# Kernel tuning notes

Hardware: AMD Instinct MI355X
Metric: run time of the kernel (lower is better)

## Reference

```python
import jax, jax.numpy as jnp
import numpy as np

D_IN = 64   # T (condition_length)
D = 128     # latent_dim
H = 8       # num_head
N = 2       # batch of graphs
M = 512     # num_nodes
T_OBS = 5.0


def leaky(v):
    return jnp.where(v >= 0, v, 0.2 * v)


def setup_inputs() -> dict:
    key = jax.random.key(0)
    ks = jax.random.split(key, 24)
    g = lambda k, s: jax.random.normal(k, s, dtype=jnp.float32) * 0.05
    return {
        "x": jax.random.normal(ks[0], (N, M, D_IN), dtype=jnp.float32),
        # f_node: T -> 2D -> D
        "fn_w1": g(ks[1], (D_IN, 2 * D)), "fn_b1": g(ks[2], (2 * D,)),
        "fn_w2": g(ks[3], (2 * D, D)),   "fn_b2": g(ks[4], (D,)),
        # per-head K/Q/V projections, stacked over heads
        "wk": g(ks[5], (H, D, D)), "bk": g(ks[6], (H, D)),
        "wq": g(ks[7], (H, D, D)), "bq": g(ks[8], (H, D)),
        "wv": g(ks[9], (H, D, D)), "bv": g(ks[10], (H, D)),
        # f_v: H*D -> D -> D
        "fv_w1": g(ks[11], (H * D, D)), "fv_b1": g(ks[12], (D,)),
        "fv_w2": g(ks[13], (D, D)),     "fv_b2": g(ks[14], (D,)),
        # f_node2edge: 2D -> D -> 1
        "fe_w1": g(ks[15], (2 * D, D)), "fe_b1": g(ks[16], (D,)),
        "fe_w2": g(ks[17], (D, 1)),     "fe_b2": g(ks[18], (1,)),
    }


def reference(x, fn_w1, fn_b1, fn_w2, fn_b2, wk, bk, wq, bq, wv, bv,
              fv_w1, fv_b1, fv_w2, fv_b2, fe_w1, fe_b1, fe_w2, fe_b2):
    n, m, T = x.shape
    # TemporalEncoding with d_hid=1: div_term = [1.0], even col -> sin(t)
    t = jnp.linspace(0.0, T_OBS, T)
    te = jnp.sin(t)  # [T]
    # f_node
    h = jax.nn.relu((x + te) @ fn_w1 + fn_b1) @ fn_w2 + fn_b2  # [N,M,D]
    # per-head attention (sender=K_i, receiver=Q_j -> scores = K Q^T)
    K = jnp.einsum('nmd,hde->hnme', h, wk) + bk[:, None, None, :]
    Q = jnp.einsum('nmd,hde->hnme', h, wq) + bq[:, None, None, :]
    V = jnp.einsum('nmd,hde->hnme', h, wv) + bv[:, None, None, :]
    scores = jnp.einsum('hnid,hnjd->hnij', K, Q)           # [H,N,M,M]
    alpha = jax.nn.softmax(leaky(scores), axis=-1)
    att = leaky(jnp.einsum('hnij,hnjd->hnid', alpha, V))   # [H,N,M,D]
    # concat heads along feature dim (head 0 first)
    att = jnp.transpose(att, (1, 2, 0, 3)).reshape(n, m, -1)  # [N,M,H*D]
    x2 = jax.nn.relu(att @ fv_w1 + fv_b1) @ fv_w2 + fv_b2 + h  # [N,M,D]
    # pairwise node2edge FFN: pair(i,j) = concat(x2_i, x2_j)
    half = fe_w1.shape[0] // 2
    A = x2 @ fe_w1[:half]   # contribution of node i
    B = x2 @ fe_w1[half:]   # contribution of node j
    hid = jax.nn.relu(A[:, :, None, :] + B[:, None, :, :] + fe_b1)  # [N,M,M,D]
    edge = (hid @ fe_w2 + fe_b2)[..., 0] / float(m)  # [N,M,M]
    return (x2, edge)
```

## Files before the change

kernel.cpp:

```cpp
#include <hip/hip_runtime.h>

typedef unsigned short u16;
typedef unsigned int u32;
typedef __attribute__((ext_vector_type(8))) short short8;
typedef __attribute__((ext_vector_type(4))) float f32x4;

__device__ __forceinline__ u16 f2b(float f) {
  union { float f; u32 i; } v; v.f = f;
  u32 i = v.i;
  return (u16)((i + 0x7FFFu + ((i >> 16) & 1u)) >> 16);
}
__device__ __forceinline__ float lo16(u32 x) { union { u32 i; float f; } v; v.i = x << 16; return v.f; }
__device__ __forceinline__ float hi16(u32 x) { union { u32 i; float f; } v; v.i = x & 0xffff0000u; return v.f; }
__device__ __forceinline__ u32 pack2(float a, float b) { return (u32)f2b(a) | ((u32)f2b(b) << 16); }

__device__ __align__(16) float g_h[1024 * 128];
__device__ __align__(16) u16   g_hb[1024 * 128];
__device__ __align__(16) u16   g_Wt[24 * 128 * 128];
__device__ __align__(16) u16   g_w1t[128 * 1024];
__device__ __align__(16) u16   g_w2t[128 * 128];
__device__ __align__(16) u16   g_fat[2 * 128 * 128];
__device__ __align__(16) u16   g_K[16 * 512 * 128];
__device__ __align__(16) u16   g_Q[16 * 512 * 128];
__device__ __align__(16) u16   g_V[16 * 512 * 128];
__device__ __align__(16) u16   g_Opb[512 * 64 * 128];
__device__ __align__(16) float g_ml[512 * 64 * 2];
__device__ __align__(16) float g_A[1024 * 128];
__device__ __align__(16) float g_Bm[1024 * 128];

__global__ void k_fnode(const float* __restrict__ x, const float* __restrict__ w1,
                        const float* __restrict__ b1, const float* __restrict__ w2,
                        const float* __restrict__ b2, const float* __restrict__ wk,
                        const float* __restrict__ wq, const float* __restrict__ wv,
                        const float* __restrict__ fvw1, const float* __restrict__ fvw2,
                        const float* __restrict__ few1) {
  __shared__ float xr[2 * 64];
  __shared__ float hids[2 * 256];
  __shared__ float red[2048];
  int tx = threadIdx.x;
  int row0 = blockIdx.x * 2;
  if (tx < 128) {
    int r = tx >> 6, k = tx & 63;
    xr[tx] = x[(row0 + r) * 64 + k] + sinf((float)k * (5.0f / 63.0f));
  }
  {
    int base = blockIdx.x * 1280 + tx;
#pragma unroll
    for (int t = 0; t < 5; t++) {
      int idx = base + t * 256;
      if (idx < 393216) {
        int ph = idx >> 14, rem = idx & 16383, e = rem >> 7, d = rem & 127;
        int proj = ph >> 3, head = ph & 7;
        const float* W = (proj == 0) ? wk : (proj == 1) ? wq : wv;
        g_Wt[idx] = f2b(W[head * 16384 + d * 128 + e]);
      } else if (idx < 524288) {
        int idx2 = idx - 393216;
        int e = idx2 >> 10, k = idx2 & 1023;
        g_w1t[idx2] = f2b(fvw1[k * 128 + e]);
      } else if (idx < 540672) {
        int idx3 = idx - 524288;
        int e = idx3 >> 7, k = idx3 & 127;
        g_w2t[idx3] = f2b(fvw2[k * 128 + e]);
      } else if (idx < 573440) {
        int idx4 = idx - 540672;
        int half = idx4 >> 14, rem = idx4 & 16383;
        int e = rem >> 7, k = rem & 127;
        g_fat[idx4] = f2b(few1[(half * 128 + k) * 128 + e]);
      }
    }
  }
  __syncthreads();
  {
    int ks = tx >> 6, cg = tx & 63;
    float acc[2][4] = {};
#pragma unroll 4
    for (int i = 0; i < 16; i++) {
      int k = ks * 16 + i;
      float4 w4 = *(const float4*)&w1[k * 256 + cg * 4];
      float a0 = xr[k], a1 = xr[64 + k];
      acc[0][0] = fmaf(a0, w4.x, acc[0][0]); acc[0][1] = fmaf(a0, w4.y, acc[0][1]);
      acc[0][2] = fmaf(a0, w4.z, acc[0][2]); acc[0][3] = fmaf(a0, w4.w, acc[0][3]);
      acc[1][0] = fmaf(a1, w4.x, acc[1][0]); acc[1][1] = fmaf(a1, w4.y, acc[1][1]);
      acc[1][2] = fmaf(a1, w4.z, acc[1][2]); acc[1][3] = fmaf(a1, w4.w, acc[1][3]);
    }
#pragma unroll
    for (int r = 0; r < 2; r++)
      *(float4*)&red[ks * 512 + r * 256 + cg * 4] = *(float4*)acc[r];
  }
  __syncthreads();
#pragma unroll
  for (int jo = 0; jo < 2; jo++) {
    int o = jo * 256 + tx;
    float s = red[o] + red[512 + o] + red[1024 + o] + red[1536 + o];
    hids[o] = fmaxf(s + b1[o & 255], 0.0f);
  }
  __syncthreads();
  {
    int ks = tx >> 5, eg = tx & 31;
    float acc[2][4] = {};
#pragma unroll 4
    for (int i = 0; i < 32; i++) {
      int k = ks * 32 + i;
      float4 w4 = *(const float4*)&w2[k * 128 + eg * 4];
      float a0 = hids[k], a1 = hids[256 + k];
      acc[0][0] = fmaf(a0, w4.x, acc[0][0]); acc[0][1] = fmaf(a0, w4.y, acc[0][1]);
      acc[0][2] = fmaf(a0, w4.z, acc[0][2]); acc[0][3] = fmaf(a0, w4.w, acc[0][3]);
      acc[1][0] = fmaf(a1, w4.x, acc[1][0]); acc[1][1] = fmaf(a1, w4.y, acc[1][1]);
      acc[1][2] = fmaf(a1, w4.z, acc[1][2]); acc[1][3] = fmaf(a1, w4.w, acc[1][3]);
    }
    __syncthreads();
#pragma unroll
    for (int r = 0; r < 2; r++)
      *(float4*)&red[ks * 256 + r * 128 + eg * 4] = *(float4*)acc[r];
  }
  __syncthreads();
  {
    float s = 0.0f;
#pragma unroll
    for (int ks = 0; ks < 8; ks++) s += red[ks * 256 + tx];
    int r = tx >> 7, e = tx & 127;
    float v = s + b2[e];
    g_h[(row0 + r) * 128 + e] = v;
    g_hb[(row0 + r) * 128 + e] = f2b(v);
  }
}

__global__ __launch_bounds__(256) void k_kqv(
    const float* __restrict__ bk, const float* __restrict__ bq,
    const float* __restrict__ bv) {
  __shared__ u16 hs[64 * 136];
  __shared__ u16 Wt[128 * 136];
  int b = blockIdx.x, tx = threadIdx.x;
  int rt = b & 15, ph = b >> 4;
  int proj = ph >> 3, head = ph & 7;
  const float* Bb = (proj == 0) ? bk : (proj == 1) ? bq : bv;
  u16* O = (proj == 0) ? g_K : (proj == 1) ? g_Q : g_V;
  int r0 = rt * 64;
#pragma unroll
  for (int t = 0; t < 4; t++) {
    int idx = t * 256 + tx, row = idx >> 4, oct = idx & 15;
    *(uint4*)&hs[row * 136 + oct * 8] = *(const uint4*)&g_hb[(r0 + row) * 128 + oct * 8];
  }
  const u16* Wtg = g_Wt + ph * 16384;
#pragma unroll
  for (int t = 0; t < 8; t++) {
    int idx = t * 256 + tx, row = idx >> 4, oct = idx & 15;
    *(uint4*)&Wt[row * 136 + oct * 8] = *(const uint4*)&Wtg[row * 128 + oct * 8];
  }
  __syncthreads();
  int lane = tx & 63, wv_ = tx >> 6, cl = lane & 15, quad = lane >> 4;
  short8 bH[4];
#pragma unroll
  for (int kk = 0; kk < 4; kk++)
    bH[kk] = *(const short8*)&hs[(wv_ * 16 + cl) * 136 + kk * 32 + quad * 8];
  f32x4 zero = {0.0f, 0.0f, 0.0f, 0.0f};
  f32x4 acc[8];
#pragma unroll
  for (int em = 0; em < 8; em++) acc[em] = zero;
#pragma unroll
  for (int em = 0; em < 8; em++)
#pragma unroll
    for (int kk = 0; kk < 4; kk++) {
      short8 aW = *(const short8*)&Wt[(em * 16 + cl) * 136 + kk * 32 + quad * 8];
      acc[em] = __builtin_amdgcn_mfma_f32_16x16x32_bf16(aW, bH[kk], acc[em], 0, 0, 0);
    }
#pragma unroll
  for (int em = 0; em < 8; em++) {
    float4 b4 = *(const float4*)&Bb[head * 128 + em * 16 + quad * 4];
    uint2 st = make_uint2(pack2(acc[em][0] + b4.x, acc[em][1] + b4.y),
                          pack2(acc[em][2] + b4.z, acc[em][3] + b4.w));
    *(uint2*)&O[(head * 1024 + r0 + wv_ * 16 + cl) * 128 + em * 16 + quad * 4] = st;
  }
}

__global__ __launch_bounds__(256) void k_attn() {
  __shared__ u16 Ks[64 * 136];
  __shared__ u16 Qs[64 * 136];
  __shared__ u16 Vt[128 * 72];
  __shared__ u16 Pw[4 * 16 * 72];
  __shared__ float alphas[4 * 16];
  int b = blockIdx.x, tx = threadIdx.x;
  int jc = b & 3, it = (b >> 2) & 7, hn = b >> 5;
  int i0 = it * 64;
  const u16* Kp = g_K + hn * 65536;
  const u16* Qp = g_Q + hn * 65536;
  const u16* Vp = g_V + hn * 65536;
#pragma unroll
  for (int t = 0; t < 4; t++) {
    int idx = t * 256 + tx, row = idx >> 4, oct = idx & 15;
    *(uint4*)&Ks[row * 136 + oct * 8] = *(const uint4*)&Kp[(i0 + row) * 128 + oct * 8];
  }
  int lane = tx & 63, wv = tx >> 6;
  int cl = lane & 15, quad = lane >> 4;
  f32x4 zero = {0.0f, 0.0f, 0.0f, 0.0f};
  f32x4 o[8];
#pragma unroll
  for (int es = 0; es < 8; es++) o[es] = zero;
  float m_ = -1e30f, l_ = 0.0f;

  for (int jt = 0; jt < 2; jt++) {
    int j0 = jc * 128 + jt * 64;
    __syncthreads();
#pragma unroll
    for (int t = 0; t < 4; t++) {
      int idx = t * 256 + tx, row = idx >> 4, oct = idx & 15;
      *(uint4*)&Qs[row * 136 + oct * 8] = *(const uint4*)&Qp[(j0 + row) * 128 + oct * 8];
    }
    {
      int jg = (tx & 15) * 4, e8 = (tx >> 4) * 8;
      uint4 r0 = *(const uint4*)&Vp[(j0 + jg + 0) * 128 + e8];
      uint4 r1 = *(const uint4*)&Vp[(j0 + jg + 1) * 128 + e8];
      uint4 r2 = *(const uint4*)&Vp[(j0 + jg + 2) * 128 + e8];
      uint4 r3 = *(const uint4*)&Vp[(j0 + jg + 3) * 128 + e8];
      const u32* p0 = (const u32*)&r0; const u32* p1 = (const u32*)&r1;
      const u32* p2 = (const u32*)&r2; const u32* p3 = (const u32*)&r3;
#pragma unroll
      for (int c = 0; c < 8; c++) {
        int w = c >> 1, sh = (c & 1) * 16;
        u32 lo = ((p0[w] >> sh) & 0xffffu) | (((p1[w] >> sh) & 0xffffu) << 16);
        u32 hi = ((p2[w] >> sh) & 0xffffu) | (((p3[w] >> sh) & 0xffffu) << 16);
        *(uint2*)&Vt[(e8 + c) * 72 + jg] = make_uint2(lo, hi);
      }
    }
    __syncthreads();
    short8 bK[4];
#pragma unroll
    for (int kk = 0; kk < 4; kk++)
      bK[kk] = *(const short8*)&Ks[(wv * 16 + cl) * 136 + kk * 32 + quad * 8];
    f32x4 st[4];
#pragma unroll
    for (int s = 0; s < 4; s++) {
      f32x4 acc = zero;
#pragma unroll
      for (int kk = 0; kk < 4; kk++) {
        short8 aQ = *(const short8*)&Qs[(s * 16 + cl) * 136 + kk * 32 + quad * 8];
        acc = __builtin_amdgcn_mfma_f32_16x16x32_bf16(aQ, bK[kk], acc, 0, 0, 0);
      }
      st[s] = acc;
    }
    float p[4][4];
    float tm = -1e30f;
#pragma unroll
    for (int s = 0; s < 4; s++)
#pragma unroll
      for (int r = 0; r < 4; r++) {
        float v = st[s][r];
        v = fmaxf(v, 0.2f * v);
        p[s][r] = v;
        tm = fmaxf(tm, v);
      }
    tm = fmaxf(tm, __shfl_xor(tm, 16));
    tm = fmaxf(tm, __shfl_xor(tm, 32));
    float mn = fmaxf(m_, tm);
    float alpha = __expf(m_ - mn);
    m_ = mn;
    float ps = 0.0f;
#pragma unroll
    for (int s = 0; s < 4; s++)
#pragma unroll
      for (int r = 0; r < 4; r++) {
        float e = __expf(p[s][r] - mn);
        p[s][r] = e;
        ps += e;
      }
    ps += __shfl_xor(ps, 16);
    ps += __shfl_xor(ps, 32);
    l_ = l_ * alpha + ps;
#pragma unroll
    for (int s = 0; s < 4; s++) {
      uint2 w2v = make_uint2(pack2(p[s][0], p[s][1]), pack2(p[s][2], p[s][3]));
      *(uint2*)&Pw[(wv * 16 + cl) * 72 + s * 16 + quad * 4] = w2v;
    }
    if (quad == 0) alphas[wv * 16 + cl] = alpha;
    __syncthreads();
    f32x4 av = *(const f32x4*)&alphas[wv * 16 + quad * 4];
#pragma unroll
    for (int es = 0; es < 8; es++) o[es] *= av;
    short8 aP[2];
#pragma unroll
    for (int k2 = 0; k2 < 2; k2++)
      aP[k2] = *(const short8*)&Pw[(wv * 16 + cl) * 72 + k2 * 32 + quad * 8];
#pragma unroll
    for (int es = 0; es < 8; es++) {
#pragma unroll
      for (int k2 = 0; k2 < 2; k2++) {
        short8 bV = *(const short8*)&Vt[(es * 16 + cl) * 72 + k2 * 32 + quad * 8];
        o[es] = __builtin_amdgcn_mfma_f32_16x16x32_bf16(aP[k2], bV, o[es], 0, 0, 0);
      }
    }
  }
#pragma unroll
  for (int es = 0; es < 8; es++)
#pragma unroll
    for (int r = 0; r < 4; r++)
      g_Opb[(b * 64 + wv * 16 + quad * 4 + r) * 128 + es * 16 + cl] = f2b(o[es][r]);
  if (quad == 0) {
    g_ml[(b * 64 + wv * 16 + cl) * 2 + 0] = m_;
    g_ml[(b * 64 + wv * 16 + cl) * 2 + 1] = l_;
  }
}

__global__ __launch_bounds__(256) void k_fv(
    const float* __restrict__ fv_b1, const float* __restrict__ fv_b2,
    const float* __restrict__ fe_b1, float* __restrict__ x2out) {
  __shared__ u16 atts[16 * 1032];
  __shared__ u16 wst[128 * 136];
  __shared__ u16 hidb[16 * 136];
  __shared__ u16 x2b[16 * 136];
  int b = blockIdx.x, tx = threadIdx.x;
  int r0 = b * 16;

  {
    int task = tx >> 1, half = tx & 1;
    int lr = task >> 3, head = task & 7;
    int gr = r0 + lr;
    int n = gr >> 9, i = gr & 511;
    int it = i >> 6, lr64 = i & 63;
    int hn = head * 2 + n;
    int mlbase = (hn * 32 + it * 4) * 64 + lr64;
    float mc[4], lc[4];
#pragma unroll
    for (int c = 0; c < 4; c++) {
      float2 ml = *(const float2*)&g_ml[(mlbase + c * 64) * 2];
      mc[c] = ml.x; lc[c] = ml.y;
    }
    float ms = fmaxf(fmaxf(mc[0], mc[1]), fmaxf(mc[2], mc[3]));
    float lsum = 0.0f;
    float ra[64];
#pragma unroll
    for (int i2 = 0; i2 < 64; i2++) ra[i2] = 0.0f;
#pragma unroll
    for (int c = 0; c < 4; c++) {
      float w = __expf(mc[c] - ms);
      lsum += w * lc[c];
      const u16* src = &g_Opb[(mlbase + c * 64) * 128 + half * 64];
#pragma unroll
      for (int ov = 0; ov < 8; ov++) {
        uint4 v = *(const uint4*)&src[ov * 8];
        ra[ov * 8 + 0] = fmaf(w, lo16(v.x), ra[ov * 8 + 0]);
        ra[ov * 8 + 1] = fmaf(w, hi16(v.x), ra[ov * 8 + 1]);
        ra[ov * 8 + 2] = fmaf(w, lo16(v.y), ra[ov * 8 + 2]);
        ra[ov * 8 + 3] = fmaf(w, hi16(v.y), ra[ov * 8 + 3]);
        ra[ov * 8 + 4] = fmaf(w, lo16(v.z), ra[ov * 8 + 4]);
        ra[ov * 8 + 5] = fmaf(w, hi16(v.z), ra[ov * 8 + 5]);
        ra[ov * 8 + 6] = fmaf(w, lo16(v.w), ra[ov * 8 + 6]);
        ra[ov * 8 + 7] = fmaf(w, hi16(v.w), ra[ov * 8 + 7]);
      }
    }
    float inv = 1.0f / lsum;
    u32 pk[32];
#pragma unroll
    for (int i2 = 0; i2 < 32; i2++) {
      float v0 = ra[i2 * 2] * inv;     v0 = fmaxf(v0, 0.2f * v0);
      float v1 = ra[i2 * 2 + 1] * inv; v1 = fmaxf(v1, 0.2f * v1);
      pk[i2] = pack2(v0, v1);
    }
    int dst = lr * 1032 + head * 128 + half * 64;
#pragma unroll
    for (int ov = 0; ov < 8; ov++)
      *(uint4*)&atts[dst + ov * 8] =
          make_uint4(pk[ov * 4], pk[ov * 4 + 1], pk[ov * 4 + 2], pk[ov * 4 + 3]);
  }
  __syncthreads();

  int lane = tx & 63, w = tx >> 6, cl = lane & 15, quad = lane >> 4;
  f32x4 zero = {0.0f, 0.0f, 0.0f, 0.0f};

  f32x4 accH[2] = {zero, zero};
  for (int kc = 0; kc < 8; kc++) {
#pragma unroll
    for (int q = 0; q < 8; q++) {
      int idx = q * 256 + tx, row = idx >> 4, oct = idx & 15;
      *(uint4*)&wst[row * 136 + oct * 8] =
          *(const uint4*)&g_w1t[row * 1024 + kc * 128 + oct * 8];
    }
    __syncthreads();
    short8 bA[4];
#pragma unroll
    for (int kk = 0; kk < 4; kk++)
      bA[kk] = *(const short8*)&atts[cl * 1032 + kc * 128 + kk * 32 + quad * 8];
#pragma unroll
    for (int t2 = 0; t2 < 2; t2++) {
      int em = 2 * w + t2;
#pragma unroll
      for (int kk = 0; kk < 4; kk++) {
        short8 aW = *(const short8*)&wst[(em * 16 + cl) * 136 + kk * 32 + quad * 8];
        accH[t2] = __builtin_amdgcn_mfma_f32_16x16x32_bf16(aW, bA[kk], accH[t2], 0, 0, 0);
      }
    }
    __syncthreads();
  }

#pragma unroll
  for (int t2 = 0; t2 < 2; t2++) {
    int eb = (2 * w + t2) * 16 + quad * 4;
    float4 b4 = *(const float4*)&fv_b1[eb];
    float v0 = fmaxf(accH[t2][0] + b4.x, 0.0f);
    float v1 = fmaxf(accH[t2][1] + b4.y, 0.0f);
    float v2 = fmaxf(accH[t2][2] + b4.z, 0.0f);
    float v3 = fmaxf(accH[t2][3] + b4.w, 0.0f);
    *(u32*)&hidb[cl * 136 + eb] = pack2(v0, v1);
    *(u32*)&hidb[cl * 136 + eb + 2] = pack2(v2, v3);
  }
#pragma unroll
  for (int q = 0; q < 8; q++) {
    int idx = q * 256 + tx, row = idx >> 4, oct = idx & 15;
    *(uint4*)&wst[row * 136 + oct * 8] = *(const uint4*)&g_w2t[row * 128 + oct * 8];
  }
  __syncthreads();

  {
    short8 bH2[4];
#pragma unroll
    for (int kk = 0; kk < 4; kk++)
      bH2[kk] = *(const short8*)&hidb[cl * 136 + kk * 32 + quad * 8];
    int gr = r0 + cl;
#pragma unroll
    for (int t2 = 0; t2 < 2; t2++) {
      int em = 2 * w + t2;
      f32x4 acc2 = zero;
#pragma unroll
      for (int kk = 0; kk < 4; kk++) {
        short8 aW = *(const short8*)&wst[(em * 16 + cl) * 136 + kk * 32 + quad * 8];
        acc2 = __builtin_amdgcn_mfma_f32_16x16x32_bf16(aW, bH2[kk], acc2, 0, 0, 0);
      }
      int eb = em * 16 + quad * 4;
      float4 b4 = *(const float4*)&fv_b2[eb];
      float4 h4 = *(const float4*)&g_h[gr * 128 + eb];
      float4 xv;
      xv.x = acc2[0] + b4.x + h4.x;
      xv.y = acc2[1] + b4.y + h4.y;
      xv.z = acc2[2] + b4.z + h4.z;
      xv.w = acc2[3] + b4.w + h4.w;
      *(float4*)&x2out[gr * 128 + eb] = xv;
      *(u32*)&x2b[cl * 136 + eb] = pack2(xv.x, xv.y);
      *(u32*)&x2b[cl * 136 + eb + 2] = pack2(xv.z, xv.w);
    }
  }
  __syncthreads();

#pragma unroll
  for (int q = 0; q < 8; q++) {
    int idx = q * 256 + tx, row = idx >> 4, oct = idx & 15;
    *(uint4*)&wst[row * 136 + oct * 8] = *(const uint4*)&g_fat[row * 128 + oct * 8];
  }
  __syncthreads();
  short8 bX[4];
#pragma unroll
  for (int kk = 0; kk < 4; kk++)
    bX[kk] = *(const short8*)&x2b[cl * 136 + kk * 32 + quad * 8];
  {
    int gr = r0 + cl;
#pragma unroll
    for (int t2 = 0; t2 < 2; t2++) {
      int em = 2 * w + t2;
      f32x4 accA = zero;
#pragma unroll
      for (int kk = 0; kk < 4; kk++) {
        short8 aW = *(const short8*)&wst[(em * 16 + cl) * 136 + kk * 32 + quad * 8];
        accA = __builtin_amdgcn_mfma_f32_16x16x32_bf16(aW, bX[kk], accA, 0, 0, 0);
      }
      int eb = em * 16 + quad * 4;
      float4 b4 = *(const float4*)&fe_b1[eb];
      float4 av;
      av.x = accA[0] + b4.x; av.y = accA[1] + b4.y;
      av.z = accA[2] + b4.z; av.w = accA[3] + b4.w;
      *(float4*)&g_A[gr * 128 + eb] = av;
    }
  }
  __syncthreads();

#pragma unroll
  for (int q = 0; q < 8; q++) {
    int idx = q * 256 + tx, row = idx >> 4, oct = idx & 15;
    *(uint4*)&wst[row * 136 + oct * 8] =
        *(const uint4*)&g_fat[16384 + row * 128 + oct * 8];
  }
  __syncthreads();
  {
    int gr = r0 + cl;
#pragma unroll
    for (int t2 = 0; t2 < 2; t2++) {
      int em = 2 * w + t2;
      f32x4 accB = zero;
#pragma unroll
      for (int kk = 0; kk < 4; kk++) {
        short8 aW = *(const short8*)&wst[(em * 16 + cl) * 136 + kk * 32 + quad * 8];
        accB = __builtin_amdgcn_mfma_f32_16x16x32_bf16(aW, bX[kk], accB, 0, 0, 0);
      }
      int eb = em * 16 + quad * 4;
      *(f32x4*)&g_Bm[gr * 128 + eb] = accB;
    }
  }
}

__global__ void k_edge(const float* __restrict__ few2, const float* __restrict__ feb2,
                       float* __restrict__ edge) {
  __shared__ float As[4 * 128];
  __shared__ float w2s[128];
  int b = blockIdx.x, tx = threadIdx.x;
  int n = b >> 8, rest = b & 255, ig = rest >> 1, jh = rest & 1;
  int i0 = ig * 4;
  if (tx < 128) w2s[tx] = few2[tx];
  As[tx] = g_A[(n * 512 + i0) * 128 + tx];
  As[tx + 256] = g_A[(n * 512 + i0) * 128 + tx + 256];
  float eb2 = feb2[0];
  __syncthreads();
  int j = jh * 256 + tx;
  const float* B0 = &g_Bm[(n * 512 + j) * 128];
  float acc[4] = {};
#pragma unroll 4
  for (int dc = 0; dc < 32; dc++) {
    float4 bv = *(const float4*)&B0[dc * 4];
    float4 w4 = *(const float4*)&w2s[dc * 4];
#pragma unroll
    for (int i = 0; i < 4; i++) {
      float4 a4 = *(const float4*)&As[i * 128 + dc * 4];
      acc[i] = fmaf(fmaxf(a4.x + bv.x, 0.0f), w4.x, acc[i]);
      acc[i] = fmaf(fmaxf(a4.y + bv.y, 0.0f), w4.y, acc[i]);
      acc[i] = fmaf(fmaxf(a4.z + bv.z, 0.0f), w4.z, acc[i]);
      acc[i] = fmaf(fmaxf(a4.w + bv.w, 0.0f), w4.w, acc[i]);
    }
  }
  const float scale = 1.0f / 512.0f;
#pragma unroll
  for (int i = 0; i < 4; i++)
    edge[(n * 512 + i0 + i) * 512 + j] = (acc[i] + eb2) * scale;
}

extern "C" void kernel_launch(void* const* d_in, const int* in_sizes, int n_in,
                              void* d_out, int out_size, void* d_ws, size_t ws_size,
                              hipStream_t stream) {
  (void)in_sizes; (void)n_in; (void)out_size; (void)d_ws; (void)ws_size;
  const float* x     = (const float*)d_in[0];
  const float* fn_w1 = (const float*)d_in[1];
  const float* fn_b1 = (const float*)d_in[2];
  const float* fn_w2 = (const float*)d_in[3];
  const float* fn_b2 = (const float*)d_in[4];
  const float* wk    = (const float*)d_in[5];
  const float* bk    = (const float*)d_in[6];
  const float* wq    = (const float*)d_in[7];
  const float* bq    = (const float*)d_in[8];
  const float* wv    = (const float*)d_in[9];
  const float* bv    = (const float*)d_in[10];
  const float* fv_w1 = (const float*)d_in[11];
  const float* fv_b1 = (const float*)d_in[12];
  const float* fv_w2 = (const float*)d_in[13];
  const float* fv_b2 = (const float*)d_in[14];
  const float* fe_w1 = (const float*)d_in[15];
  const float* fe_b1 = (const float*)d_in[16];
  const float* fe_w2 = (const float*)d_in[17];
  const float* fe_b2 = (const float*)d_in[18];

  float* x2out = (float*)d_out;
  float* edge  = x2out + 131072;

  k_fnode<<<512, 256, 0, stream>>>(x, fn_w1, fn_b1, fn_w2, fn_b2, wk, wq, wv,
                                   fv_w1, fv_w2, fe_w1);
  k_kqv<<<384, 256, 0, stream>>>(bk, bq, bv);
  k_attn<<<512, 256, 0, stream>>>();
  k_fv<<<64, 256, 0, stream>>>(fv_b1, fv_b2, fe_b1, x2out);
  k_edge<<<512, 256, 0, stream>>>(fe_w2, fe_b2, edge);
}
```

Measured before the change: 144.1 us.

## Fuse K/Q/V projection into attention kernel and widen fv kernel to 512 threads

Removes the separate K/Q/V projection kernel. The attention kernel now computes its K tile, and the Q and V tiles for each j-chunk, directly from bf16 h and the weights into shared memory, which drops the K/Q/V global round trip and one launch. The price is recomputation: Q and V are projected once per i-tile (8x redundant) and K once per j-chunk (4x). The fv kernel moves to 512 threads with one 16-column tile per wave and reads weights straight from global memory instead of staging them through shared memory, cutting syncs.

```diff
diff --git a/kernel.cpp b/kernel.cpp
--- a/kernel.cpp
+++ b/kernel.cpp
@@ -20,9 +20,6 @@
 __device__ __align__(16) u16   g_w1t[128 * 1024];
 __device__ __align__(16) u16   g_w2t[128 * 128];
 __device__ __align__(16) u16   g_fat[2 * 128 * 128];
-__device__ __align__(16) u16   g_K[16 * 512 * 128];
-__device__ __align__(16) u16   g_Q[16 * 512 * 128];
-__device__ __align__(16) u16   g_V[16 * 512 * 128];
 __device__ __align__(16) u16   g_Opb[512 * 64 * 128];
 __device__ __align__(16) float g_ml[512 * 64 * 2];
 __device__ __align__(16) float g_A[1024 * 128];
@@ -125,74 +122,53 @@
   }
 }
 
-__global__ __launch_bounds__(256) void k_kqv(
+__global__ __launch_bounds__(256) void k_qattn(
     const float* __restrict__ bk, const float* __restrict__ bq,
     const float* __restrict__ bv) {
-  __shared__ u16 hs[64 * 136];
-  __shared__ u16 Wt[128 * 136];
-  int b = blockIdx.x, tx = threadIdx.x;
-  int rt = b & 15, ph = b >> 4;
-  int proj = ph >> 3, head = ph & 7;
-  const float* Bb = (proj == 0) ? bk : (proj == 1) ? bq : bv;
-  u16* O = (proj == 0) ? g_K : (proj == 1) ? g_Q : g_V;
-  int r0 = rt * 64;
-#pragma unroll
-  for (int t = 0; t < 4; t++) {
-    int idx = t * 256 + tx, row = idx >> 4, oct = idx & 15;
-    *(uint4*)&hs[row * 136 + oct * 8] = *(const uint4*)&g_hb[(r0 + row) * 128 + oct * 8];
-  }
-  const u16* Wtg = g_Wt + ph * 16384;
-#pragma unroll
-  for (int t = 0; t < 8; t++) {
-    int idx = t * 256 + tx, row = idx >> 4, oct = idx & 15;
-    *(uint4*)&Wt[row * 136 + oct * 8] = *(const uint4*)&Wtg[row * 128 + oct * 8];
-  }
-  __syncthreads();
-  int lane = tx & 63, wv_ = tx >> 6, cl = lane & 15, quad = lane >> 4;
-  short8 bH[4];
-#pragma unroll
-  for (int kk = 0; kk < 4; kk++)
-    bH[kk] = *(const short8*)&hs[(wv_ * 16 + cl) * 136 + kk * 32 + quad * 8];
-  f32x4 zero = {0.0f, 0.0f, 0.0f, 0.0f};
-  f32x4 acc[8];
-#pragma unroll
-  for (int em = 0; em < 8; em++) acc[em] = zero;
-#pragma unroll
-  for (int em = 0; em < 8; em++)
-#pragma unroll
-    for (int kk = 0; kk < 4; kk++) {
-      short8 aW = *(const short8*)&Wt[(em * 16 + cl) * 136 + kk * 32 + quad * 8];
-      acc[em] = __builtin_amdgcn_mfma_f32_16x16x32_bf16(aW, bH[kk], acc[em], 0, 0, 0);
-    }
-#pragma unroll
-  for (int em = 0; em < 8; em++) {
-    float4 b4 = *(const float4*)&Bb[head * 128 + em * 16 + quad * 4];
-    uint2 st = make_uint2(pack2(acc[em][0] + b4.x, acc[em][1] + b4.y),
-                          pack2(acc[em][2] + b4.z, acc[em][3] + b4.w));
-    *(uint2*)&O[(head * 1024 + r0 + wv_ * 16 + cl) * 128 + em * 16 + quad * 4] = st;
-  }
-}
-
-__global__ __launch_bounds__(256) void k_attn() {
-  __shared__ u16 Ks[64 * 136];
+  __shared__ union { u16 Ks[64 * 136]; u16 Pw[64 * 72]; } kp;
   __shared__ u16 Qs[64 * 136];
   __shared__ u16 Vt[128 * 72];
-  __shared__ u16 Pw[4 * 16 * 72];
-  __shared__ float alphas[4 * 16];
+  __shared__ float alphas[64];
   int b = blockIdx.x, tx = threadIdx.x;
   int jc = b & 3, it = (b >> 2) & 7, hn = b >> 5;
+  int head = hn >> 1, n = hn & 1;
   int i0 = it * 64;
-  const u16* Kp = g_K + hn * 65536;
-  const u16* Qp = g_Q + hn * 65536;
-  const u16* Vp = g_V + hn * 65536;
-#pragma unroll
-  for (int t = 0; t < 4; t++) {
-    int idx = t * 256 + tx, row = idx >> 4, oct = idx & 15;
-    *(uint4*)&Ks[row * 136 + oct * 8] = *(const uint4*)&Kp[(i0 + row) * 128 + oct * 8];
-  }
-  int lane = tx & 63, wv = tx >> 6;
-  int cl = lane & 15, quad = lane >> 4;
+  int lane = tx & 63, wv = tx >> 6, cl = lane & 15, quad = lane >> 4;
+  const u16* WtK = g_Wt + (head) * 16384;
+  const u16* WtQ = g_Wt + (8 + head) * 16384;
+  const u16* WtV = g_Wt + (16 + head) * 16384;
   f32x4 zero = {0.0f, 0.0f, 0.0f, 0.0f};
+
+  {
+    const u16* hbK = &g_hb[(n * 512 + i0 + wv * 16 + cl) * 128];
+    short8 bH[4];
+#pragma unroll
+    for (int kk = 0; kk < 4; kk++)
+      bH[kk] = *(const short8*)&hbK[kk * 32 + quad * 8];
+    f32x4 acc[8];
+#pragma unroll
+    for (int em = 0; em < 8; em++) acc[em] = zero;
+#pragma unroll
+    for (int em = 0; em < 8; em++)
+#pragma unroll
+      for (int kk = 0; kk < 4; kk++) {
+        short8 aW = *(const short8*)&WtK[(em * 16 + cl) * 128 + kk * 32 + quad * 8];
+        acc[em] = __builtin_amdgcn_mfma_f32_16x16x32_bf16(aW, bH[kk], acc[em], 0, 0, 0);
+      }
+#pragma unroll
+    for (int em = 0; em < 8; em++) {
+      float4 b4 = *(const float4*)&bk[head * 128 + em * 16 + quad * 4];
+      int addr = (wv * 16 + cl) * 136 + em * 16 + quad * 4;
+      *(u32*)&kp.Ks[addr] = pack2(acc[em][0] + b4.x, acc[em][1] + b4.y);
+      *(u32*)&kp.Ks[addr + 2] = pack2(acc[em][2] + b4.z, acc[em][3] + b4.w);
+    }
+  }
+  __syncthreads();
+  short8 bK[4];
+#pragma unroll
+  for (int kk = 0; kk < 4; kk++)
+    bK[kk] = *(const short8*)&kp.Ks[(wv * 16 + cl) * 136 + kk * 32 + quad * 8];
+
   f32x4 o[8];
 #pragma unroll
   for (int es = 0; es < 8; es++) o[es] = zero;
@@ -201,32 +177,57 @@
   for (int jt = 0; jt < 2; jt++) {
     int j0 = jc * 128 + jt * 64;
     __syncthreads();
-#pragma unroll
-    for (int t = 0; t < 4; t++) {
-      int idx = t * 256 + tx, row = idx >> 4, oct = idx & 15;
-      *(uint4*)&Qs[row * 136 + oct * 8] = *(const uint4*)&Qp[(j0 + row) * 128 + oct * 8];
-    }
     {
-      int jg = (tx & 15) * 4, e8 = (tx >> 4) * 8;
-      uint4 r0 = *(const uint4*)&Vp[(j0 + jg + 0) * 128 + e8];
-      uint4 r1 = *(const uint4*)&Vp[(j0 + jg + 1) * 128 + e8];
-      uint4 r2 = *(const uint4*)&Vp[(j0 + jg + 2) * 128 + e8];
-      uint4 r3 = *(const uint4*)&Vp[(j0 + jg + 3) * 128 + e8];
-      const u32* p0 = (const u32*)&r0; const u32* p1 = (const u32*)&r1;
-      const u32* p2 = (const u32*)&r2; const u32* p3 = (const u32*)&r3;
-#pragma unroll
-      for (int c = 0; c < 8; c++) {
-        int w = c >> 1, sh = (c & 1) * 16;
-        u32 lo = ((p0[w] >> sh) & 0xffffu) | (((p1[w] >> sh) & 0xffffu) << 16);
-        u32 hi = ((p2[w] >> sh) & 0xffffu) | (((p3[w] >> sh) & 0xffffu) << 16);
-        *(uint2*)&Vt[(e8 + c) * 72 + jg] = make_uint2(lo, hi);
+      const u16* hbQ = &g_hb[(n * 512 + j0 + wv * 16 + cl) * 128];
+      short8 bH[4];
+#pragma unroll
+      for (int kk = 0; kk < 4; kk++)
+        bH[kk] = *(const short8*)&hbQ[kk * 32 + quad * 8];
+      f32x4 acc[8];
+#pragma unroll
+      for (int em = 0; em < 8; em++) acc[em] = zero;
+#pragma unroll
+      for (int em = 0; em < 8; em++)
+#pragma unroll
+        for (int kk = 0; kk < 4; kk++) {
+          short8 aW = *(const short8*)&WtQ[(em * 16 + cl) * 128 + kk * 32 + quad * 8];
+          acc[em] = __builtin_amdgcn_mfma_f32_16x16x32_bf16(aW, bH[kk], acc[em], 0, 0, 0);
+        }
+#pragma unroll
+      for (int em = 0; em < 8; em++) {
+        float4 b4 = *(const float4*)&bq[head * 128 + em * 16 + quad * 4];
+        int addr = (wv * 16 + cl) * 136 + em * 16 + quad * 4;
+        *(u32*)&Qs[addr] = pack2(acc[em][0] + b4.x, acc[em][1] + b4.y);
+        *(u32*)&Qs[addr + 2] = pack2(acc[em][2] + b4.z, acc[em][3] + b4.w);
+      }
+    }
+    {
+      const u16* hbV = &g_hb[(n * 512 + j0 + wv * 16 + cl) * 128];
+      short8 bH[4];
+#pragma unroll
+      for (int kk = 0; kk < 4; kk++)
+        bH[kk] = *(const short8*)&hbV[kk * 32 + quad * 8];
+      f32x4 acc[8];
+#pragma unroll
+      for (int em = 0; em < 8; em++) acc[em] = zero;
+#pragma unroll
+      for (int em = 0; em < 8; em++)
+#pragma unroll
+        for (int kk = 0; kk < 4; kk++) {
+          short8 aW = *(const short8*)&WtV[(em * 16 + cl) * 128 + kk * 32 + quad * 8];
+          acc[em] = __builtin_amdgcn_mfma_f32_16x16x32_bf16(aW, bH[kk], acc[em], 0, 0, 0);
+        }
+      int jl = wv * 16 + cl;
+#pragma unroll
+      for (int em = 0; em < 8; em++) {
+        float4 b4 = *(const float4*)&bv[head * 128 + em * 16 + quad * 4];
+        Vt[(em * 16 + quad * 4 + 0) * 72 + jl] = f2b(acc[em][0] + b4.x);
+        Vt[(em * 16 + quad * 4 + 1) * 72 + jl] = f2b(acc[em][1] + b4.y);
+        Vt[(em * 16 + quad * 4 + 2) * 72 + jl] = f2b(acc[em][2] + b4.z);
+        Vt[(em * 16 + quad * 4 + 3) * 72 + jl] = f2b(acc[em][3] + b4.w);
       }
     }
     __syncthreads();
-    short8 bK[4];
-#pragma unroll
-    for (int kk = 0; kk < 4; kk++)
-      bK[kk] = *(const short8*)&Ks[(wv * 16 + cl) * 136 + kk * 32 + quad * 8];
     f32x4 st[4];
 #pragma unroll
     for (int s = 0; s < 4; s++) {
@@ -269,7 +270,7 @@
 #pragma unroll
     for (int s = 0; s < 4; s++) {
       uint2 w2v = make_uint2(pack2(p[s][0], p[s][1]), pack2(p[s][2], p[s][3]));
-      *(uint2*)&Pw[(wv * 16 + cl) * 72 + s * 16 + quad * 4] = w2v;
+      *(uint2*)&kp.Pw[(wv * 16 + cl) * 72 + s * 16 + quad * 4] = w2v;
     }
     if (quad == 0) alphas[wv * 16 + cl] = alpha;
     __syncthreads();
@@ -279,7 +280,7 @@
     short8 aP[2];
 #pragma unroll
     for (int k2 = 0; k2 < 2; k2++)
-      aP[k2] = *(const short8*)&Pw[(wv * 16 + cl) * 72 + k2 * 32 + quad * 8];
+      aP[k2] = *(const short8*)&kp.Pw[(wv * 16 + cl) * 72 + k2 * 32 + quad * 8];
 #pragma unroll
     for (int es = 0; es < 8; es++) {
 #pragma unroll
@@ -300,18 +301,17 @@
   }
 }
 
-__global__ __launch_bounds__(256) void k_fv(
+__global__ __launch_bounds__(512) void k_fv(
     const float* __restrict__ fv_b1, const float* __restrict__ fv_b2,
     const float* __restrict__ fe_b1, float* __restrict__ x2out) {
   __shared__ u16 atts[16 * 1032];
-  __shared__ u16 wst[128 * 136];
   __shared__ u16 hidb[16 * 136];
   __shared__ u16 x2b[16 * 136];
   int b = blockIdx.x, tx = threadIdx.x;
   int r0 = b * 16;
 
   {
-    int task = tx >> 1, half = tx & 1;
+    int task = tx >> 2, q4 = tx & 3;
     int lr = task >> 3, head = task & 7;
     int gr = r0 + lr;
     int n = gr >> 9, i = gr & 511;
@@ -326,16 +326,16 @@
     }
     float ms = fmaxf(fmaxf(mc[0], mc[1]), fmaxf(mc[2], mc[3]));
     float lsum = 0.0f;
-    float ra[64];
-#pragma unroll
-    for (int i2 = 0; i2 < 64; i2++) ra[i2] = 0.0f;
+    float ra[32];
+#pragma unroll
+    for (int i2 = 0; i2 < 32; i2++) ra[i2] = 0.0f;
 #pragma unroll
     for (int c = 0; c < 4; c++) {
       float w = __expf(mc[c] - ms);
       lsum += w * lc[c];
-      const u16* src = &g_Opb[(mlbase + c * 64) * 128 + half * 64];
-#pragma unroll
-      for (int ov = 0; ov < 8; ov++) {
+      const u16* src = &g_Opb[(mlbase + c * 64) * 128 + q4 * 32];
+#pragma unroll
+      for (int ov = 0; ov < 4; ov++) {
         uint4 v = *(const uint4*)&src[ov * 8];
         ra[ov * 8 + 0] = fmaf(w, lo16(v.x), ra[ov * 8 + 0]);
         ra[ov * 8 + 1] = fmaf(w, hi16(v.x), ra[ov * 8 + 1]);
@@ -348,16 +348,16 @@
       }
     }
     float inv = 1.0f / lsum;
-    u32 pk[32];
-#pragma unroll
-    for (int i2 = 0; i2 < 32; i2++) {
+    u32 pk[16];
+#pragma unroll
+    for (int i2 = 0; i2 < 16; i2++) {
       float v0 = ra[i2 * 2] * inv;     v0 = fmaxf(v0, 0.2f * v0);
       float v1 = ra[i2 * 2 + 1] * inv; v1 = fmaxf(v1, 0.2f * v1);
       pk[i2] = pack2(v0, v1);
     }
-    int dst = lr * 1032 + head * 128 + half * 64;
-#pragma unroll
-    for (int ov = 0; ov < 8; ov++)
+    int dst = lr * 1032 + head * 128 + q4 * 32;
+#pragma unroll
+    for (int ov = 0; ov < 4; ov++)
       *(uint4*)&atts[dst + ov * 8] =
           make_uint4(pk[ov * 4], pk[ov * 4 + 1], pk[ov * 4 + 2], pk[ov * 4 + 3]);
   }
@@ -366,131 +366,76 @@
   int lane = tx & 63, w = tx >> 6, cl = lane & 15, quad = lane >> 4;
   f32x4 zero = {0.0f, 0.0f, 0.0f, 0.0f};
 
-  f32x4 accH[2] = {zero, zero};
+  f32x4 accH = zero;
+#pragma unroll 2
   for (int kc = 0; kc < 8; kc++) {
-#pragma unroll
-    for (int q = 0; q < 8; q++) {
-      int idx = q * 256 + tx, row = idx >> 4, oct = idx & 15;
-      *(uint4*)&wst[row * 136 + oct * 8] =
-          *(const uint4*)&g_w1t[row * 1024 + kc * 128 + oct * 8];
-    }
-    __syncthreads();
     short8 bA[4];
 #pragma unroll
     for (int kk = 0; kk < 4; kk++)
       bA[kk] = *(const short8*)&atts[cl * 1032 + kc * 128 + kk * 32 + quad * 8];
 #pragma unroll
-    for (int t2 = 0; t2 < 2; t2++) {
-      int em = 2 * w + t2;
-#pragma unroll
-      for (int kk = 0; kk < 4; kk++) {
-        short8 aW = *(const short8*)&wst[(em * 16 + cl) * 136 + kk * 32 + quad * 8];
-        accH[t2] = __builtin_amdgcn_mfma_f32_16x16x32_bf16(aW, bA[kk], accH[t2], 0, 0, 0);
-      }
-    }
-    __syncthreads();
-  }
-
-#pragma unroll
-  for (int t2 = 0; t2 < 2; t2++) {
-    int eb = (2 * w + t2) * 16 + quad * 4;
+    for (int kk = 0; kk < 4; kk++) {
+      short8 aW = *(const short8*)&g_w1t[(w * 16 + cl) * 1024 + kc * 128 + kk * 32 + quad * 8];
+      accH = __builtin_amdgcn_mfma_f32_16x16x32_bf16(aW, bA[kk], accH, 0, 0, 0);
+    }
+  }
+  {
+    int eb = w * 16 + quad * 4;
     float4 b4 = *(const float4*)&fv_b1[eb];
-    float v0 = fmaxf(accH[t2][0] + b4.x, 0.0f);
-    float v1 = fmaxf(accH[t2][1] + b4.y, 0.0f);
-    float v2 = fmaxf(accH[t2][2] + b4.z, 0.0f);
-    float v3 = fmaxf(accH[t2][3] + b4.w, 0.0f);
+    float v0 = fmaxf(accH[0] + b4.x, 0.0f);
+    float v1 = fmaxf(accH[1] + b4.y, 0.0f);
+    float v2 = fmaxf(accH[2] + b4.z, 0.0f);
+    float v3 = fmaxf(accH[3] + b4.w, 0.0f);
     *(u32*)&hidb[cl * 136 + eb] = pack2(v0, v1);
     *(u32*)&hidb[cl * 136 + eb + 2] = pack2(v2, v3);
   }
-#pragma unroll
-  for (int q = 0; q < 8; q++) {
-    int idx = q * 256 + tx, row = idx >> 4, oct = idx & 15;
-    *(uint4*)&wst[row * 136 + oct * 8] = *(const uint4*)&g_w2t[row * 128 + oct * 8];
-  }
-  __syncthreads();
-
+  __syncthreads();
   {
     short8 bH2[4];
 #pragma unroll
     for (int kk = 0; kk < 4; kk++)
       bH2[kk] = *(const short8*)&hidb[cl * 136 + kk * 32 + quad * 8];
     int gr = r0 + cl;
-#pragma unroll
-    for (int t2 = 0; t2 < 2; t2++) {
-      int em = 2 * w + t2;
-      f32x4 acc2 = zero;
-#pragma unroll
-      for (int kk = 0; kk < 4; kk++) {
-        short8 aW = *(const short8*)&wst[(em * 16 + cl) * 136 + kk * 32 + quad * 8];
-        acc2 = __builtin_amdgcn_mfma_f32_16x16x32_bf16(aW, bH2[kk], acc2, 0, 0, 0);
-      }
-      int eb = em * 16 + quad * 4;
-      float4 b4 = *(const float4*)&fv_b2[eb];
-      float4 h4 = *(const float4*)&g_h[gr * 128 + eb];
-      float4 xv;
-      xv.x = acc2[0] + b4.x + h4.x;
-      xv.y = acc2[1] + b4.y + h4.y;
-      xv.z = acc2[2] + b4.z + h4.z;
-      xv.w = acc2[3] + b4.w + h4.w;
-      *(float4*)&x2out[gr * 128 + eb] = xv;
-      *(u32*)&x2b[cl * 136 + eb] = pack2(xv.x, xv.y);
-      *(u32*)&x2b[cl * 136 + eb + 2] = pack2(xv.z, xv.w);
-    }
-  }
-  __syncthreads();
-
-#pragma unroll
-  for (int q = 0; q < 8; q++) {
-    int idx = q * 256 + tx, row = idx >> 4, oct = idx & 15;
-    *(uint4*)&wst[row * 136 + oct * 8] = *(const uint4*)&g_fat[row * 128 + oct * 8];
-  }
-  __syncthreads();
-  short8 bX[4];
-#pragma unroll
-  for (int kk = 0; kk < 4; kk++)
-    bX[kk] = *(const short8*)&x2b[cl * 136 + kk * 32 + quad * 8];
-  {
+    f32x4 acc2 = zero;
+#pragma unroll
+    for (int kk = 0; kk < 4; kk++) {
+      short8 aW = *(const short8*)&g_w2t[(w * 16 + cl) * 128 + kk * 32 + quad * 8];
+      acc2 = __builtin_amdgcn_mfma_f32_16x16x32_bf16(aW, bH2[kk], acc2, 0, 0, 0);
+    }
+    int eb = w * 16 + quad * 4;
+    float4 b4 = *(const float4*)&fv_b2[eb];
+    float4 h4 = *(const float4*)&g_h[gr * 128 + eb];
+    float4 xv;
+    xv.x = acc2[0] + b4.x + h4.x;
+    xv.y = acc2[1] + b4.y + h4.y;
+    xv.z = acc2[2] + b4.z + h4.z;
+    xv.w = acc2[3] + b4.w + h4.w;
+    *(float4*)&x2out[gr * 128 + eb] = xv;
+    *(u32*)&x2b[cl * 136 + eb] = pack2(xv.x, xv.y);
+    *(u32*)&x2b[cl * 136 + eb + 2] = pack2(xv.z, xv.w);
+  }
+  __syncthreads();
+  {
+    short8 bX[4];
+#pragma unroll
+    for (int kk = 0; kk < 4; kk++)
+      bX[kk] = *(const short8*)&x2b[cl * 136 + kk * 32 + quad * 8];
     int gr = r0 + cl;
-#pragma unroll
-    for (int t2 = 0; t2 < 2; t2++) {
-      int em = 2 * w + t2;
-      f32x4 accA = zero;
-#pragma unroll
-      for (int kk = 0; kk < 4; kk++) {
-        short8 aW = *(const short8*)&wst[(em * 16 + cl) * 136 + kk * 32 + quad * 8];
-        accA = __builtin_amdgcn_mfma_f32_16x16x32_bf16(aW, bX[kk], accA, 0, 0, 0);
-      }
-      int eb = em * 16 + quad * 4;
-      float4 b4 = *(const float4*)&fe_b1[eb];
-      float4 av;
-      av.x = accA[0] + b4.x; av.y = accA[1] + b4.y;
-      av.z = accA[2] + b4.z; av.w = accA[3] + b4.w;
-      *(float4*)&g_A[gr * 128 + eb] = av;
-    }
-  }
-  __syncthreads();
-
-#pragma unroll
-  for (int q = 0; q < 8; q++) {
-    int idx = q * 256 + tx, row = idx >> 4, oct = idx & 15;
-    *(uint4*)&wst[row * 136 + oct * 8] =
-        *(const uint4*)&g_fat[16384 + row * 128 + oct * 8];
-  }
-  __syncthreads();
-  {
-    int gr = r0 + cl;
-#pragma unroll
-    for (int t2 = 0; t2 < 2; t2++) {
-      int em = 2 * w + t2;
-      f32x4 accB = zero;
-#pragma unroll
-      for (int kk = 0; kk < 4; kk++) {
-        short8 aW = *(const short8*)&wst[(em * 16 + cl) * 136 + kk * 32 + quad * 8];
-        accB = __builtin_amdgcn_mfma_f32_16x16x32_bf16(aW, bX[kk], accB, 0, 0, 0);
-      }
-      int eb = em * 16 + quad * 4;
-      *(f32x4*)&g_Bm[gr * 128 + eb] = accB;
-    }
+    f32x4 accA = zero, accB = zero;
+#pragma unroll
+    for (int kk = 0; kk < 4; kk++) {
+      short8 aWA = *(const short8*)&g_fat[(w * 16 + cl) * 128 + kk * 32 + quad * 8];
+      short8 aWB = *(const short8*)&g_fat[16384 + (w * 16 + cl) * 128 + kk * 32 + quad * 8];
+      accA = __builtin_amdgcn_mfma_f32_16x16x32_bf16(aWA, bX[kk], accA, 0, 0, 0);
+      accB = __builtin_amdgcn_mfma_f32_16x16x32_bf16(aWB, bX[kk], accB, 0, 0, 0);
+    }
+    int eb = w * 16 + quad * 4;
+    float4 b4 = *(const float4*)&fe_b1[eb];
+    float4 av;
+    av.x = accA[0] + b4.x; av.y = accA[1] + b4.y;
+    av.z = accA[2] + b4.z; av.w = accA[3] + b4.w;
+    *(float4*)&g_A[gr * 128 + eb] = av;
+    *(f32x4*)&g_Bm[gr * 128 + eb] = accB;
   }
 }
 
@@ -557,8 +502,7 @@
 
   k_fnode<<<512, 256, 0, stream>>>(x, fn_w1, fn_b1, fn_w2, fn_b2, wk, wq, wv,
                                    fv_w1, fv_w2, fe_w1);
-  k_kqv<<<384, 256, 0, stream>>>(bk, bq, bv);
-  k_attn<<<512, 256, 0, stream>>>();
-  k_fv<<<64, 256, 0, stream>>>(fv_b1, fv_b2, fe_b1, x2out);
+  k_qattn<<<512, 256, 0, stream>>>(bk, bq, bv);
+  k_fv<<<64, 512, 0, stream>>>(fv_b1, fv_b2, fe_b1, x2out);
   k_edge<<<512, 256, 0, stream>>>(fe_w2, fe_b2, edge);
 }
```

Measured after the change: 179.6 us. 1.25x slower.
